# Kernel optimization log

Hardware: AMD Instinct MI355X
Metric: run time of the kernel (lower is better)

The kernel has to match this reference:

```python
import jax, jax.numpy as jnp
from jax import lax
import numpy as np

NUM_EMBEDDINGS = 512
EMBEDDING_DIM = 64
COMMITMENT_COST = 0.25
SPARSITY_LEVEL = 8


def batch_omp(data, dictionary, max_nonzero):
    """Batch-OMP (Rubinstein et al.).
    data: [D, N], dictionary: [D, K] (columns unit-norm). Returns gamma [K, N].
    Runs a fixed max_nonzero greedy steps (the torch tolerance 1e-7 never
    triggers early exit on random data).
    """
    D, N = data.shape
    K = dictionary.shape[1]
    G = dictionary.T @ dictionary                 # [K, K] Gram matrix
    h_bar = (dictionary.T @ data).T               # [N, K] initial correlations
    h = h_bar
    mask = jnp.zeros((N, K), dtype=bool)          # selected-atom indicator
    rows = jnp.arange(N)
    L = jnp.ones((N, 1, 1), dtype=data.dtype)     # incremental Cholesky of G[I,I]
    I = None                                      # [N, k] selected indices
    x = jnp.zeros((N, K), dtype=data.dtype)
    for k in range(1, max_nonzero + 1):
        # greedy atom selection (masking already-chosen atoms)
        idx = jnp.argmax(jnp.abs(h * (~mask).astype(h.dtype)), axis=1)   # [N]
        mask = mask.at[rows, idx].set(True)
        if k > 1:
            g = G[I, idx[:, None]][..., None]                            # [N, k-1, 1]
            w = lax.linalg.triangular_solve(L, g, left_side=True, lower=True)
            w = jnp.swapaxes(w, 1, 2)                                    # [N, 1, k-1]
            w_corner = jnp.sqrt(1.0 - jnp.sum(w * w, axis=2, keepdims=True))
            top = jnp.concatenate([L, jnp.zeros((N, k - 1, 1), L.dtype)], axis=2)
            bot = jnp.concatenate([w, w_corner], axis=2)
            L = jnp.concatenate([top, bot], axis=1)                      # [N, k, k]
            I = jnp.concatenate([I, idx[:, None]], axis=1)
        else:
            I = idx[:, None]
        hb = jnp.take_along_axis(h_bar, I, axis=1)[..., None]            # [N, k, 1]
        # cholesky_solve: L L^T x = hb
        y = lax.linalg.triangular_solve(L, hb, left_side=True, lower=True)
        xs = lax.linalg.triangular_solve(L, y, left_side=True, lower=True,
                                         transpose_a=True)              # [N, k, 1]
        x = jnp.zeros((N, K), data.dtype).at[rows[:, None], I].set(xs[..., 0])
        beta = x @ G                                                     # x is zero off-support
        h = h_bar - beta
    return x.T                                                           # [K, N]


def setup_inputs() -> dict:
    key = jax.random.key(0)
    k1, k2 = jax.random.split(key)
    z_e = jax.random.normal(k1, (32, EMBEDDING_DIM, 32, 32), dtype=jnp.float32)
    dictionary = jax.random.normal(k2, (EMBEDDING_DIM, NUM_EMBEDDINGS), dtype=jnp.float32)
    beta = jnp.array([1.0 - COMMITMENT_COST], dtype=jnp.float32)  # nn.Parameter(1 - commitment_cost)
    return {"z_e": z_e, "dictionary": dictionary, "beta": beta}


def reference(z_e, dictionary, beta):
    # straight-through column normalization (torch does it via .data assignment)
    Dn_val = dictionary / jnp.linalg.norm(dictionary, axis=0)
    Dn = dictionary + lax.stop_gradient(Dn_val - dictionary)
    zp = jnp.transpose(z_e, (0, 2, 3, 1))                 # [B, H, W, C]
    ze_shape = zp.shape
    zf = zp.reshape(EMBEDDING_DIM, -1)                    # view(D, -1): [D, N]
    gamma = lax.stop_gradient(batch_omp(zf, Dn, SPARSITY_LEVEL))   # [K, N]; copied via .data in torch
    recon = Dn @ gamma                                    # [D, N]
    e_latent_loss = jnp.mean((lax.stop_gradient(recon) - zf) ** 2)
    q_loss = jnp.mean((recon - lax.stop_gradient(zf)) ** 2)
    loss = e_latent_loss * COMMITMENT_COST + beta[0] * q_loss
    recon_st = zf + lax.stop_gradient(recon - zf)         # straight-through
    sm = jax.nn.softmax(gamma, axis=0)
    perplexity = jnp.exp(-jnp.mean(jnp.sum(sm * jnp.log(sm + 1e-10), axis=0)))
    recon_out = jnp.transpose(recon_st.reshape(ze_shape), (0, 3, 1, 2))
    return loss, recon_out, lax.stop_gradient(zf), perplexity, gamma
```

## Files before the change

### kernel.cpp

```cpp
#include <hip/hip_runtime.h>
#include <math.h>

#define NCOL 32768
#define KAT  512
#define DIM  64

#define O_LOSS  0
#define O_RECON 1
#define O_ZF    2097153
#define O_PERP  4194305
#define O_GAMMA 4194306

#define WS_DN   0
#define WS_DNT  32768
#define WS_G    65536
#define WS_ACC  327680

__global__ void prep_kernel(const float* __restrict__ dict, float* __restrict__ ws) {
    float* Dn  = ws + WS_DN;
    float* DnT = ws + WS_DNT;
    float* acc = ws + WS_ACC;
    int a = threadIdx.x;
    if (a < 2) acc[a] = 0.f;
    float s = 0.f;
    #pragma unroll
    for (int d = 0; d < DIM; ++d) { float v = dict[d*KAT + a]; s += v * v; }
    float nrm = sqrtf(s);
    #pragma unroll
    for (int d = 0; d < DIM; ++d) {
        float v = dict[d*KAT + a] / nrm;
        Dn[d*KAT + a]  = v;
        DnT[a*DIM + d] = v;
    }
}

__global__ void gram_kernel(const float* __restrict__ ws_in, float* __restrict__ ws) {
    const float* Dn = ws_in + WS_DN;
    float* G = ws + WS_G;
    int i = blockIdx.x, j = threadIdx.x;
    float s = 0.f;
    #pragma unroll
    for (int d = 0; d < DIM; ++d)
        s = fmaf(Dn[d*KAT + i], Dn[d*KAT + j], s);
    G[i*KAT + j] = s;
}

__global__ __launch_bounds__(256) void zf_kernel(const float* __restrict__ z_e,
                                                 float* __restrict__ out) {
    __shared__ float tile[64 * 33];
    int s = blockIdx.x;
    int b = s >> 5, h = s & 31;
    int t = threadIdx.x;
    int srcbase = b * 65536 + h * 32;
    #pragma unroll
    for (int i = 0; i < 8; ++i) {
        int e = t + i * 256;
        int c = e >> 5, w = e & 31;
        tile[c * 33 + w] = z_e[srcbase + c * 1024 + w];
    }
    __syncthreads();
    int obase = O_ZF + s * 2048;
    #pragma unroll
    for (int i = 0; i < 8; ++i) {
        int e = t + i * 256;
        out[obase + e] = tile[(e & 63) * 33 + (e >> 6)];
    }
}

__global__ void gzero_kernel(float2* __restrict__ g2) {
    int id = blockIdx.x * 256 + threadIdx.x;
    #pragma unroll
    for (int i = 0; i < 4; ++i)
        g2[id + i * 2097152] = make_float2(0.f, 0.f);
}

__global__ __launch_bounds__(256) void omp_kernel(const float* __restrict__ z_e,
                                                  const float* __restrict__ ws,
                                                  float* __restrict__ out,
                                                  float* __restrict__ wsw) {
    const float* Dn  = ws + WS_DN;
    const float* DnT = ws + WS_DNT;
    const float* G   = ws + WS_G;
    float* acc = wsw + WS_ACC;

    __shared__ float xcols[DIM * 16];
    __shared__ float hbar[16 * KAT];

    const int t = threadIdx.x;
    const int n_base = blockIdx.x * 16;

    #pragma unroll
    for (int i = 0; i < 4; ++i) {
        int e = t + i * 256;
        int d = e >> 4, c = e & 15;
        int L = d * NCOL + n_base + c;
        int src = (L >> 16) * 65536 + (L & 63) * 1024 + (((L >> 11) & 31) << 5) + ((L >> 6) & 31);
        xcols[e] = z_e[src];
    }
    __syncthreads();

    {
        float a0[16], a1[16];
        #pragma unroll
        for (int i = 0; i < 16; ++i) { a0[i] = 0.f; a1[i] = 0.f; }
        const float4* xc4 = (const float4*)xcols;
        for (int d = 0; d < DIM; ++d) {
            float v0 = Dn[d * KAT + t];
            float v1 = Dn[d * KAT + 256 + t];
            #pragma unroll
            for (int q = 0; q < 4; ++q) {
                float4 xv = xc4[d * 4 + q];
                a0[q*4+0] = fmaf(v0, xv.x, a0[q*4+0]);
                a0[q*4+1] = fmaf(v0, xv.y, a0[q*4+1]);
                a0[q*4+2] = fmaf(v0, xv.z, a0[q*4+2]);
                a0[q*4+3] = fmaf(v0, xv.w, a0[q*4+3]);
                a1[q*4+0] = fmaf(v1, xv.x, a1[q*4+0]);
                a1[q*4+1] = fmaf(v1, xv.y, a1[q*4+1]);
                a1[q*4+2] = fmaf(v1, xv.z, a1[q*4+2]);
                a1[q*4+3] = fmaf(v1, xv.w, a1[q*4+3]);
            }
        }
        #pragma unroll
        for (int c = 0; c < 16; ++c) {
            hbar[c * KAT + t]       = a0[c];
            hbar[c * KAT + 256 + t] = a1[c];
        }
    }
    __syncthreads();

    const int wv = t >> 6, lane = t & 63;
    float wv_sq = 0.f, wv_S = 0.f;

    #pragma unroll 1
    for (int cc = 0; cc < 4; ++cc) {
        const int col = wv * 4 + cc;
        const int n = n_base + col;
        const float* hbcol = hbar + col * KAT;

        float h[8];
        #pragma unroll
        for (int r = 0; r < 8; ++r) h[r] = hbcol[(r << 6) + lane];

        unsigned msk = 0;
        float uv[56];
        float Lr[28];
        float invd[8], yv[8], xr[8];
        int Iv[8];

        #pragma unroll
        for (int k = 0; k < 8; ++k) {
            float bv = -1.f; int bi = 0;
            #pragma unroll
            for (int r = 0; r < 8; ++r) {
                float av = ((msk >> r) & 1) ? -1.f : fabsf(h[r]);
                if (av > bv) { bv = av; bi = (r << 6) | lane; }
            }
            unsigned long long key = (bv >= 0.f)
                ? ((((unsigned long long)__float_as_uint(bv)) << 32) | (unsigned)(511 - bi))
                : 0ull;
            #pragma unroll
            for (int off = 32; off; off >>= 1) {
                unsigned long long ok = __shfl_xor(key, off, 64);
                if (ok > key) key = ok;
            }
            const int idx = 511 - (int)(key & 511u);
            if ((idx & 63) == lane) msk |= 1u << (idx >> 6);

            const float* grow = G + idx * KAT;

            float gk[8];
            if (k < 7) {
                #pragma unroll
                for (int r = 0; r < 8; ++r) gk[r] = grow[(r << 6) + lane];
            }

            if (k == 0) {
                invd[0] = 1.f;
            } else {
                float w[7];
                #pragma unroll
                for (int i = 0; i < 7; ++i) if (i < k) {
                    float a = grow[Iv[i]];
                    #pragma unroll
                    for (int j = 0; j < 7; ++j) if (j < i) a -= Lr[i*(i-1)/2 + j] * w[j];
                    w[i] = a * invd[i];
                }
                float s2 = 0.f;
                #pragma unroll
                for (int j = 0; j < 7; ++j) if (j < k) { Lr[k*(k-1)/2 + j] = w[j]; s2 += w[j]*w[j]; }
                invd[k] = 1.f / sqrtf(1.f - s2);
            }
            Iv[k] = idx;

            {
                float a = hbcol[idx];
                #pragma unroll
                for (int j = 0; j < 7; ++j) if (j < k) a -= Lr[k*(k-1)/2 + j] * yv[j];
                yv[k] = a * invd[k];
            }

            if (k < 7) {
                #pragma unroll
                for (int r = 0; r < 8; ++r) {
                    float a = gk[r];
                    #pragma unroll
                    for (int j = 0; j < 7; ++j) if (j < k) a -= Lr[k*(k-1)/2 + j] * uv[j*8 + r];
                    a *= invd[k];
                    uv[k*8 + r] = a;
                    h[r] -= yv[k] * a;
                }
            }
        }

        #pragma unroll
        for (int i = 7; i >= 0; --i) {
            float a = yv[i];
            #pragma unroll
            for (int j = 0; j < 8; ++j) if (j > i) a -= Lr[j*(j-1)/2 + i] * xr[j];
            xr[i] = a * invd[i];
        }

        #pragma unroll
        for (int j = 0; j < 8; ++j)
            if (lane == j) out[O_GAMMA + Iv[j] * NCOL + n] = xr[j];

        float rec = 0.f;
        #pragma unroll
        for (int j = 0; j < 8; ++j)
            rec = fmaf(xr[j], DnT[Iv[j] * DIM + lane], rec);
        int L = lane * NCOL + n;
        int perm = (L >> 16) * 65536 + (L & 63) * 1024 + (((L >> 11) & 31) << 5) + ((L >> 6) & 31);
        out[O_RECON + perm] = rec;

        float xd = xcols[lane * 16 + col];
        float diff = rec - xd;
        float sq = diff * diff;
        #pragma unroll
        for (int off = 32; off; off >>= 1) sq += __shfl_xor(sq, off, 64);
        if (lane == 0) wv_sq += sq;

        if (lane == 0) {
            float m = 0.f;
            #pragma unroll
            for (int j = 0; j < 8; ++j) m = fmaxf(m, xr[j]);
            float e0 = expf(-m);
            float Z = 504.f * e0;
            float es[8];
            #pragma unroll
            for (int j = 0; j < 8; ++j) { es[j] = expf(xr[j] - m); Z += es[j]; }
            float invZ = 1.f / Z;
            float p0 = e0 * invZ;
            float S = 504.f * p0 * logf(p0 + 1e-10f);
            #pragma unroll
            for (int j = 0; j < 8; ++j) { float p = es[j] * invZ; S += p * logf(p + 1e-10f); }
            wv_S += S;
        }
    }

    if (lane == 0) {
        atomicAdd(&acc[0], wv_sq);
        atomicAdd(&acc[1], wv_S);
    }
}

__global__ void fin_kernel(const float* __restrict__ ws, const float* __restrict__ beta,
                           float* __restrict__ out) {
    const float* acc = ws + WS_ACC;
    float mse = acc[0] / 2097152.f;
    out[O_LOSS] = mse * 0.25f + beta[0] * mse;
    out[O_PERP] = expf(-acc[1] / 32768.f);
}

extern "C" void kernel_launch(void* const* d_in, const int* in_sizes, int n_in,
                              void* d_out, int out_size, void* d_ws, size_t ws_size,
                              hipStream_t stream) {
    const float* z_e  = (const float*)d_in[0];
    const float* dict = (const float*)d_in[1];
    const float* beta = (const float*)d_in[2];
    float* out = (float*)d_out;
    float* ws  = (float*)d_ws;

    prep_kernel<<<1, 512, 0, stream>>>(dict, ws);
    gram_kernel<<<512, 512, 0, stream>>>(ws, ws);
    zf_kernel<<<1024, 256, 0, stream>>>(z_e, out);
    gzero_kernel<<<8192, 256, 0, stream>>>((float2*)(out + O_GAMMA));
    omp_kernel<<<2048, 256, 0, stream>>>(z_e, ws, out, ws);
    fin_kernel<<<1, 1, 0, stream>>>(ws, beta, out);
}
```

Measured before the change: 381.0 us.

## Derive Cholesky row from stored projections and halve columns per block

Each new Cholesky row is now read from the already-computed projection vectors uv through a wave shuffle. This replaces re-solving a triangular system with scattered G loads. The current correlation h at the chosen atom is likewise shuffled in, so the hbar reload and forward substitution are gone. Blocks now handle 8 columns instead of 16, with launch_bounds hinting 4 blocks per CU and a transposed shared copy for conflict-free residual reads. This trades more blocks and repeated Dn reads for lower shared memory use and a shorter serial dependency chain per step.

```diff
diff --git a/kernel.cpp b/kernel.cpp
--- a/kernel.cpp
+++ b/kernel.cpp
@@ -74,42 +74,45 @@
         g2[id + i * 2097152] = make_float2(0.f, 0.f);
 }
 
-__global__ __launch_bounds__(256) void omp_kernel(const float* __restrict__ z_e,
-                                                  const float* __restrict__ ws,
-                                                  float* __restrict__ out,
-                                                  float* __restrict__ wsw) {
+__global__ __launch_bounds__(256, 4) void omp_kernel(const float* __restrict__ z_e,
+                                                     const float* __restrict__ ws,
+                                                     float* __restrict__ out,
+                                                     float* __restrict__ wsw) {
     const float* Dn  = ws + WS_DN;
     const float* DnT = ws + WS_DNT;
     const float* G   = ws + WS_G;
     float* acc = wsw + WS_ACC;
 
-    __shared__ float xcols[DIM * 16];
-    __shared__ float hbar[16 * KAT];
+    __shared__ float xcols[DIM * 8];
+    __shared__ float xcolsT[8 * DIM];
+    __shared__ float hbar[8 * KAT];
 
     const int t = threadIdx.x;
-    const int n_base = blockIdx.x * 16;
-
-    #pragma unroll
-    for (int i = 0; i < 4; ++i) {
+    const int n_base = blockIdx.x * 8;
+
+    #pragma unroll
+    for (int i = 0; i < 2; ++i) {
         int e = t + i * 256;
-        int d = e >> 4, c = e & 15;
+        int d = e >> 3, c = e & 7;
         int L = d * NCOL + n_base + c;
         int src = (L >> 16) * 65536 + (L & 63) * 1024 + (((L >> 11) & 31) << 5) + ((L >> 6) & 31);
-        xcols[e] = z_e[src];
+        float v = z_e[src];
+        xcols[e] = v;
+        xcolsT[c * DIM + d] = v;
     }
     __syncthreads();
 
     {
-        float a0[16], a1[16];
-        #pragma unroll
-        for (int i = 0; i < 16; ++i) { a0[i] = 0.f; a1[i] = 0.f; }
+        float a0[8], a1[8];
+        #pragma unroll
+        for (int i = 0; i < 8; ++i) { a0[i] = 0.f; a1[i] = 0.f; }
         const float4* xc4 = (const float4*)xcols;
         for (int d = 0; d < DIM; ++d) {
             float v0 = Dn[d * KAT + t];
             float v1 = Dn[d * KAT + 256 + t];
             #pragma unroll
-            for (int q = 0; q < 4; ++q) {
-                float4 xv = xc4[d * 4 + q];
+            for (int q = 0; q < 2; ++q) {
+                float4 xv = xc4[d * 2 + q];
                 a0[q*4+0] = fmaf(v0, xv.x, a0[q*4+0]);
                 a0[q*4+1] = fmaf(v0, xv.y, a0[q*4+1]);
                 a0[q*4+2] = fmaf(v0, xv.z, a0[q*4+2]);
@@ -121,7 +124,7 @@
             }
         }
         #pragma unroll
-        for (int c = 0; c < 16; ++c) {
+        for (int c = 0; c < 8; ++c) {
             hbar[c * KAT + t]       = a0[c];
             hbar[c * KAT + 256 + t] = a1[c];
         }
@@ -132,8 +135,8 @@
     float wv_sq = 0.f, wv_S = 0.f;
 
     #pragma unroll 1
-    for (int cc = 0; cc < 4; ++cc) {
-        const int col = wv * 4 + cc;
+    for (int cc = 0; cc < 2; ++cc) {
+        const int col = wv * 2 + cc;
         const int n = n_base + col;
         const float* hbcol = hbar + col * KAT;
 
@@ -164,50 +167,48 @@
                 if (ok > key) key = ok;
             }
             const int idx = 511 - (int)(key & 511u);
-            if ((idx & 63) == lane) msk |= 1u << (idx >> 6);
+            const int rwin = idx >> 6, lwin = idx & 63;
+            if (lwin == lane) msk |= 1u << rwin;
+            Iv[k] = idx;
 
             const float* grow = G + idx * KAT;
-
             float gk[8];
             if (k < 7) {
                 #pragma unroll
                 for (int r = 0; r < 8; ++r) gk[r] = grow[(r << 6) + lane];
             }
 
-            if (k == 0) {
-                invd[0] = 1.f;
-            } else {
-                float w[7];
+            float hsel = h[0];
+            #pragma unroll
+            for (int r = 1; r < 8; ++r) if (rwin == r) hsel = h[r];
+            float hwin = __shfl(hsel, lwin, 64);
+
+            float Lk[7];
+            #pragma unroll
+            for (int j = 0; j < 7; ++j) if (j < k) {
+                float us = uv[j*8 + 0];
                 #pragma unroll
-                for (int i = 0; i < 7; ++i) if (i < k) {
-                    float a = grow[Iv[i]];
-                    #pragma unroll
-                    for (int j = 0; j < 7; ++j) if (j < i) a -= Lr[i*(i-1)/2 + j] * w[j];
-                    w[i] = a * invd[i];
-                }
-                float s2 = 0.f;
-                #pragma unroll
-                for (int j = 0; j < 7; ++j) if (j < k) { Lr[k*(k-1)/2 + j] = w[j]; s2 += w[j]*w[j]; }
-                invd[k] = 1.f / sqrtf(1.f - s2);
-            }
-            Iv[k] = idx;
-
-            {
-                float a = hbcol[idx];
-                #pragma unroll
-                for (int j = 0; j < 7; ++j) if (j < k) a -= Lr[k*(k-1)/2 + j] * yv[j];
-                yv[k] = a * invd[k];
-            }
+                for (int r = 1; r < 8; ++r) if (rwin == r) us = uv[j*8 + r];
+                Lk[j] = __shfl(us, lwin, 64);
+            }
+            float s2 = 0.f;
+            #pragma unroll
+            for (int j = 0; j < 7; ++j) if (j < k) {
+                Lr[k*(k-1)/2 + j] = Lk[j];
+                s2 += Lk[j] * Lk[j];
+            }
+            invd[k] = (k == 0) ? 1.f : 1.f / sqrtf(1.f - s2);
+            yv[k] = hwin * invd[k];
 
             if (k < 7) {
                 #pragma unroll
                 for (int r = 0; r < 8; ++r) {
                     float a = gk[r];
                     #pragma unroll
-                    for (int j = 0; j < 7; ++j) if (j < k) a -= Lr[k*(k-1)/2 + j] * uv[j*8 + r];
+                    for (int j = 0; j < 7; ++j) if (j < k) a = fmaf(-Lk[j], uv[j*8 + r], a);
                     a *= invd[k];
                     uv[k*8 + r] = a;
-                    h[r] -= yv[k] * a;
+                    h[r] = fmaf(-yv[k], a, h[r]);
                 }
             }
         }
@@ -216,7 +217,7 @@
         for (int i = 7; i >= 0; --i) {
             float a = yv[i];
             #pragma unroll
-            for (int j = 0; j < 8; ++j) if (j > i) a -= Lr[j*(j-1)/2 + i] * xr[j];
+            for (int j = 0; j < 8; ++j) if (j > i) a = fmaf(-Lr[j*(j-1)/2 + i], xr[j], a);
             xr[i] = a * invd[i];
         }
 
@@ -232,7 +233,7 @@
         int perm = (L >> 16) * 65536 + (L & 63) * 1024 + (((L >> 11) & 31) << 5) + ((L >> 6) & 31);
         out[O_RECON + perm] = rec;
 
-        float xd = xcols[lane * 16 + col];
+        float xd = xcolsT[col * DIM + lane];
         float diff = rec - xd;
         float sq = diff * diff;
         #pragma unroll
@@ -284,6 +285,6 @@
     gram_kernel<<<512, 512, 0, stream>>>(ws, ws);
     zf_kernel<<<1024, 256, 0, stream>>>(z_e, out);
     gzero_kernel<<<8192, 256, 0, stream>>>((float2*)(out + O_GAMMA));
-    omp_kernel<<<2048, 256, 0, stream>>>(z_e, ws, out, ws);
+    omp_kernel<<<4096, 256, 0, stream>>>(z_e, ws, out, ws);
     fin_kernel<<<1, 1, 0, stream>>>(ws, beta, out);
 }
```

Result: slower. 566.2 us (+48.6%).
